# Kernel optimization log

Measured on AMD Instinct MI355X. Metric: run time of the kernel, lower is better.

The kernel has to match this reference:

```python
import jax, jax.numpy as jnp
import numpy as np
from jax import lax

CAP_SIZE = 8
N_IN, N_OUT, OUT_SIZE = 144, 10, 16
ROUTING_ITERS = 3
DN = ('NCHW', 'OIHW', 'NCHW')


def setup_inputs() -> dict:
    key = jax.random.key(0)
    ks = jax.random.split(key, 6)
    B = 2048
    inp = {
        'input': jax.random.uniform(ks[0], (B, 1, 28, 28), dtype=jnp.float32),
        'conv1_w': jax.random.normal(ks[1], (16, 1, 9, 9), dtype=jnp.float32) * 0.1,
        'conv1_b': jnp.zeros((16,), dtype=jnp.float32),
        'conv2_w': jax.random.normal(ks[2], (32, 16, 9, 9), dtype=jnp.float32) * 0.05,
        'conv2_b': jnp.zeros((32,), dtype=jnp.float32),
        'W_route': jax.random.normal(ks[3], (N_IN, N_OUT, OUT_SIZE, CAP_SIZE), dtype=jnp.float32) * 0.1,
    }
    return inp


def squash(s, axis=-1, eps=1e-8):
    sq = jnp.sum(jnp.square(s), axis=axis, keepdims=True)
    return (sq / (1.0 + sq)) * s / jnp.sqrt(sq + eps)


def reference(input, conv1_w, conv1_b, conv2_w, conv2_b, W_route):
    # PrimaryCaps: two valid convs
    x = lax.conv_general_dilated(input, conv1_w, (1, 1), 'VALID', dimension_numbers=DN)
    x = x + conv1_b[None, :, None, None]                      # [B,16,20,20]
    x = lax.conv_general_dilated(x, conv2_w, (2, 2), 'VALID', dimension_numbers=DN)
    x = x + conv2_b[None, :, None, None]                      # [B,32,6,6]
    B = x.shape[0]
    u = jnp.transpose(x.reshape(B, CAP_SIZE, -1), (0, 2, 1))  # [B,144,8]

    # prediction vectors u_hat[b,i,j,:] = W[i,j] @ u[b,i]
    u_hat = jnp.einsum('iojc,bic->bioj', W_route, u)          # [B,144,10,16]

    # routing-by-agreement
    b_log = jnp.zeros((B, N_IN, N_OUT), dtype=u_hat.dtype)
    for _ in range(ROUTING_ITERS):
        c = jax.nn.softmax(b_log, axis=2)                     # couple over out caps
        s = jnp.einsum('bio,biod->bod', c, u_hat)             # [B,10,16]
        v = squash(s)                                         # [B,10,16]
        b_log = b_log + jnp.einsum('biod,bod->bio', u_hat, v)

    pred = jnp.sqrt(jnp.sum(jnp.square(v), axis=-1))          # [B,10]
    return (pred, v)
```

## Files before the change

kernel.cpp:

```cpp
#include <hip/hip_runtime.h>


typedef _Float16 half2_t __attribute__((ext_vector_type(2)));
typedef _Float16 f16x4 __attribute__((ext_vector_type(4)));
typedef _Float16 f16x8 __attribute__((ext_vector_type(8)));
typedef float f32x16 __attribute__((ext_vector_type(16)));

static __device__ __forceinline__ float fdot2f(half2_t a, half2_t b, float c) {
#if __has_builtin(__builtin_amdgcn_fdot2)
  return __builtin_amdgcn_fdot2(a, b, c, false);
#else
  return c + (float)a[0] * (float)b[0] + (float)a[1] * (float)b[1];
#endif
}

static __device__ __forceinline__ half2_t h2(unsigned int u) {
  return __builtin_bit_cast(half2_t, u);
}

static __device__ __forceinline__ unsigned int pkh2(float a, float b) {
  half2_t h;
  h[0] = (_Float16)a;
  h[1] = (_Float16)b;
  return __builtin_bit_cast(unsigned int, h);
}

static __device__ __forceinline__ f32x16 zero16() {
  f32x16 z = {0.f, 0.f, 0.f, 0.f, 0.f, 0.f, 0.f, 0.f,
              0.f, 0.f, 0.f, 0.f, 0.f, 0.f, 0.f, 0.f};
  return z;
}

__global__ __launch_bounds__(256) void packAll(
    const float* __restrict__ w2, const float* __restrict__ Wr,
    _Float16* __restrict__ wBg, unsigned int* __restrict__ wPr) {
  int idx = blockIdx.x * 256 + threadIdx.x;
  if (idx < 92160) {
    int cp = idx & 3;
    int row = idx >> 2;
    const float* src = Wr + (size_t)row * 8 + cp * 2;
    wPr[idx] = pkh2(src[0], src[1]);
  }
  if (idx < 41472) {
    int j = idx & 7;
    int lane = (idx >> 3) & 63;
    int step = idx >> 9;
    int kh = step / 9, kw = step - kh * 9;
    int co = lane & 31, ci = (lane >> 5) * 8 + j;
    wBg[idx] = (_Float16)w2[(co * 16 + ci) * 81 + kh * 9 + kw];
  }
}

__global__ __launch_bounds__(320) void conv_fused(
    const float* __restrict__ in, const float* __restrict__ w,
    const float* __restrict__ bias1, const _Float16* __restrict__ wBg,
    const float* __restrict__ bias2, float* __restrict__ u) {
  __shared__ __align__(16) float sIn[784];
  __shared__ float sW[1296];
  __shared__ __align__(16) _Float16 sOut[8000];
  int b = blockIdx.x, t = threadIdx.x;
  const float* inb = in + b * 784;
  for (int i = t; i < 784; i += 320) sIn[i] = inb[i];
  for (int i = t; i < 1296; i += 320) sW[i] = w[i];
  __syncthreads();
  {
    int co = t / 20, oh = t % 20;
    float bv = bias1[co];
    float acc[20];
#pragma unroll
    for (int j = 0; j < 20; ++j) acc[j] = bv;
#pragma unroll
    for (int kh = 0; kh < 9; ++kh) {
      float r[28];
      const float4* row = (const float4*)&sIn[(oh + kh) * 28];
#pragma unroll
      for (int q = 0; q < 7; ++q) {
        float4 v = row[q];
        r[q * 4 + 0] = v.x; r[q * 4 + 1] = v.y; r[q * 4 + 2] = v.z; r[q * 4 + 3] = v.w;
      }
      const float* wr = &sW[co * 81 + kh * 9];
#pragma unroll
      for (int kw = 0; kw < 9; ++kw) {
        float wv = wr[kw];
#pragma unroll
        for (int j = 0; j < 20; ++j) acc[j] += wv * r[kw + j];
      }
    }
#pragma unroll
    for (int j = 0; j < 20; ++j) sOut[(oh * 20 + j) * 20 + co] = (_Float16)acc[j];
  }
  __syncthreads();

  int wv = t >> 6, lane = t & 63;
  if (wv < 2) {
    int l31 = lane & 31, half = lane >> 5;
    int r = wv * 32 + l31;
    int rc = (r < 36) ? r : 35;
    int oh = rc / 6, ow = rc - oh * 6;
    int tb = (oh * 40 + ow * 2) * 20 + half * 8;
    f32x16 acc = zero16();
    for (int kh = 0; kh < 9; ++kh) {
      int abase = tb + kh * 400;
#pragma unroll
      for (int kw = 0; kw < 9; ++kw) {
        f16x8 bf = *(const f16x8*)(wBg + ((kh * 9 + kw) * 64 + lane) * 8);
        const _Float16* ap = sOut + abase + kw * 20;
        f16x4 lo = *(const f16x4*)ap;
        f16x4 hi = *(const f16x4*)(ap + 4);
        f16x8 a = __builtin_shufflevector(lo, hi, 0, 1, 2, 3, 4, 5, 6, 7);
        acc = __builtin_amdgcn_mfma_f32_32x32x16_f16(a, bf, acc, 0, 0, 0);
      }
    }
    float bv = bias2[l31];
    int c8 = l31 >> 2;
    int ibco = (l31 & 3) * 36;
    float* ub = u + (size_t)b * 1152;
#pragma unroll
    for (int reg = 0; reg < 16; ++reg) {
      int rr = wv * 32 + (reg & 3) + 8 * (reg >> 2) + 4 * half;
      if (rr < 36) ub[(ibco + rr) * 8 + c8] = acc[reg] + bv;
    }
  }
}

__global__ __launch_bounds__(1024) void routing2_kernel(
    const float* __restrict__ u, const unsigned int* __restrict__ wPr,
    float* __restrict__ out, int B) {
  __shared__ unsigned int uhh[2][11808];
  __shared__ unsigned int ush[2][576];
  __shared__ float blog[2][1440];
  __shared__ float cc[2][1440];
  __shared__ float spart[2][960];
  __shared__ float ss[2][160];
  __shared__ float vv[2][160];
  __shared__ unsigned int vvh[2][80];
  int b0 = blockIdx.x * 2, t = threadIdx.x;
  for (int j = t; j < 1152; j += 1024) {
    int sl2 = j / 576, k = j - sl2 * 576;
    float2 p = *(const float2*)(u + (size_t)(b0 + sl2) * 1152 + k * 2);
    ush[sl2][k] = pkh2(p.x, p.y);
  }
  for (int j = t; j < 2880; j += 1024) blog[j / 1440][j % 1440] = 0.f;
  __syncthreads();

  {
    const uint4* W4 = (const uint4*)wPr;
    int idx = t;
    bool valid = idx < 11520;
    int i_ = 0, dp_ = 0;
    uint4 w0a, w1a;
    if (valid) {
      i_ = idx / 80; dp_ = idx - i_ * 80;
      int row = i_ * 160 + (dp_ >> 3) * 16 + (dp_ & 7) * 2;
      w0a = W4[row]; w1a = W4[row + 1];
    }
    while (valid) {
      int nidx = idx + 1024;
      bool nvalid = nidx < 11520;
      int ni = 0, ndp = 0;
      uint4 w0b, w1b;
      if (nvalid) {
        ni = nidx / 80; ndp = nidx - ni * 80;
        int nrow = ni * 160 + (ndp >> 3) * 16 + (ndp & 7) * 2;
        w0b = W4[nrow]; w1b = W4[nrow + 1];
      }
#pragma unroll
      for (int sl2 = 0; sl2 < 2; ++sl2) {
        const uint2* up = (const uint2*)&ush[sl2][i_ * 4];
        uint2 ua = up[0], ub = up[1];
        half2_t u0 = h2(ua.x), u1 = h2(ua.y), u2 = h2(ub.x), u3 = h2(ub.y);
        float a0 = fdot2f(h2(w0a.x), u0,
                   fdot2f(h2(w0a.y), u1,
                   fdot2f(h2(w0a.z), u2, fdot2f(h2(w0a.w), u3, 0.f))));
        float a1 = fdot2f(h2(w1a.x), u0,
                   fdot2f(h2(w1a.y), u1,
                   fdot2f(h2(w1a.z), u2, fdot2f(h2(w1a.w), u3, 0.f))));
        uhh[sl2][i_ * 82 + dp_] = pkh2(a0, a1);
      }
      idx = nidx; i_ = ni; dp_ = ndp;
      w0a = w0b; w1a = w1b;
      valid = nvalid;
    }
  }
  __syncthreads();

  int sl = t >> 9, tl = t & 511;
  for (int it = 0; it < 3; ++it) {
    if (it > 0) {
      if (tl < 144) {
        const float* br = &blog[sl][tl * 10];
        float mx = br[0];
#pragma unroll
        for (int o = 1; o < 10; ++o) mx = fmaxf(mx, br[o]);
        float e[10];
        float sum = 0.f;
#pragma unroll
        for (int o = 0; o < 10; ++o) { e[o] = __expf(br[o] - mx); sum += e[o]; }
        float inv = 1.0f / sum;
#pragma unroll
        for (int o = 0; o < 10; ++o) cc[sl][tl * 10 + o] = e[o] * inv;
      }
      __syncthreads();
    }
    if (tl < 480) {
      int ch = tl / 80, dp = tl - ch * 80;
      int o = dp >> 3;
      float a0 = 0.f, a1 = 0.f;
      int i0 = ch * 24;
      if (it == 0) {
        for (int i = i0; i < i0 + 24; ++i) {
          half2_t h = h2(uhh[sl][i * 82 + dp]);
          a0 += (float)h[0]; a1 += (float)h[1];
        }
      } else {
        for (int i = i0; i < i0 + 24; ++i) {
          float c = cc[sl][i * 10 + o];
          half2_t h = h2(uhh[sl][i * 82 + dp]);
          a0 += c * (float)h[0]; a1 += c * (float)h[1];
        }
      }
      spart[sl][ch * 160 + dp * 2] = a0;
      spart[sl][ch * 160 + dp * 2 + 1] = a1;
    }
    __syncthreads();
    if (tl < 160) {
      float s = 0.f;
#pragma unroll
      for (int ch = 0; ch < 6; ++ch) s += spart[sl][ch * 160 + tl];
      ss[sl][tl] = (it == 0) ? s * 0.1f : s;
    }
    __syncthreads();
    if (tl < 10) {
      float sq = 0.f;
#pragma unroll
      for (int d = 0; d < 16; ++d) { float x = ss[sl][tl * 16 + d]; sq += x * x; }
      float coef = (sq / (1.0f + sq)) / sqrtf(sq + 1e-8f);
#pragma unroll
      for (int q = 0; q < 8; ++q) {
        float v0 = coef * ss[sl][tl * 16 + 2 * q];
        float v1 = coef * ss[sl][tl * 16 + 2 * q + 1];
        vv[sl][tl * 16 + 2 * q] = v0;
        vv[sl][tl * 16 + 2 * q + 1] = v1;
        vvh[sl][tl * 8 + q] = pkh2(v0, v1);
      }
      if (it == 2) out[(b0 + sl) * 10 + tl] = coef * sqrtf(sq);
    }
    __syncthreads();
    if (it < 2) {
      for (int idx = t; idx < 2880; idx += 1024) {
        int s2 = idx / 1440, r = idx - s2 * 1440;
        int i = r / 10, o = r - i * 10;
        const uint2* uhp = (const uint2*)&uhh[s2][i * 82 + o * 8];
        const uint2* vp = (const uint2*)&vvh[s2][o * 8];
        float dot = 0.f;
#pragma unroll
        for (int q = 0; q < 4; ++q) {
          uint2 A = uhp[q], V = vp[q];
          dot = fdot2f(h2(A.x), h2(V.x), fdot2f(h2(A.y), h2(V.y), dot));
        }
        blog[s2][r] += dot;
      }
      __syncthreads();
    }
  }
  if (tl < 160) out[B * 10 + (b0 + sl) * 160 + tl] = vv[sl][tl];
}

extern "C" void kernel_launch(void* const* d_in, const int* in_sizes, int n_in,
                              void* d_out, int out_size, void* d_ws, size_t ws_size,
                              hipStream_t stream) {
  const float* in = (const float*)d_in[0];
  const float* w1 = (const float*)d_in[1];
  const float* b1 = (const float*)d_in[2];
  const float* w2 = (const float*)d_in[3];
  const float* b2 = (const float*)d_in[4];
  const float* Wr = (const float*)d_in[5];
  float* out = (float*)d_out;
  int B = in_sizes[0] / 784;
  float* wsf = (float*)d_ws;

  float* u = wsf;
  float* tail = wsf + (size_t)B * 1152;
  _Float16* wBg = (_Float16*)tail;
  unsigned int* wPr = (unsigned int*)(tail + 20736);

  packAll<<<360, 256, 0, stream>>>(w2, Wr, wBg, wPr);
  conv_fused<<<B, 320, 0, stream>>>(in, w1, b1, wBg, b2, u);
  routing2_kernel<<<B / 2, 1024, 0, stream>>>(u, wPr, out, B);
}
```

Before: 110.1 us.

## Fuse conv and dynamic routing into one per-sample kernel with aliased LDS

Merges the conv kernel and the routing kernel into a single kernel with one block of 320 threads per sample. The primary-capsule vector u stays in shared memory as fp16 instead of round-tripping through global memory, which removes one launch. Shared memory is one byte buffer with overlapping regions so the conv scratch is reused for the u_hat and routing arrays. In exchange, routing now runs on 320 threads per sample instead of 512, and the larger LDS footprint may limit how many blocks fit per CU.

Result: slower. 161.3 us (+46.4%).

```diff
diff --git a/kernel.cpp b/kernel.cpp
--- a/kernel.cpp
+++ b/kernel.cpp
@@ -51,18 +51,30 @@
   }
 }
 
-__global__ __launch_bounds__(320) void conv_fused(
-    const float* __restrict__ in, const float* __restrict__ w,
+__global__ __launch_bounds__(320) void capsnet_fused(
+    const float* __restrict__ in, const float* __restrict__ w1g,
     const float* __restrict__ bias1, const _Float16* __restrict__ wBg,
-    const float* __restrict__ bias2, float* __restrict__ u) {
-  __shared__ __align__(16) float sIn[784];
-  __shared__ float sW[1296];
-  __shared__ __align__(16) _Float16 sOut[8000];
+    const float* __restrict__ bias2, const unsigned int* __restrict__ wPr,
+    float* __restrict__ out, int B) {
+  __shared__ __align__(16) unsigned char smem[65216];
+  float* sIn = (float*)smem;
+  float* sW = (float*)(smem + 3136);
+  float* blog = (float*)smem;
+  float* cc = (float*)(smem + 5760);
+  _Float16* sOut = (_Float16*)(smem + 11520);
+  unsigned int* uhh = (unsigned int*)(smem + 11520);
+  _Float16* uu = (_Float16*)(smem + 58752);
+  float* spart = (float*)(smem + 61056);
+  float* ss = (float*)(smem + 63616);
+  float* vv = (float*)(smem + 64256);
+  unsigned int* vvh = (unsigned int*)(smem + 64896);
+
   int b = blockIdx.x, t = threadIdx.x;
   const float* inb = in + b * 784;
   for (int i = t; i < 784; i += 320) sIn[i] = inb[i];
-  for (int i = t; i < 1296; i += 320) sW[i] = w[i];
-  __syncthreads();
+  for (int i = t; i < 1296; i += 320) sW[i] = w1g[i];
+  __syncthreads();
+
   {
     int co = t / 20, oh = t % 20;
     float bv = bias1[co];
@@ -76,7 +88,8 @@
 #pragma unroll
       for (int q = 0; q < 7; ++q) {
         float4 v = row[q];
-        r[q * 4 + 0] = v.x; r[q * 4 + 1] = v.y; r[q * 4 + 2] = v.z; r[q * 4 + 3] = v.w;
+        r[q * 4 + 0] = v.x; r[q * 4 + 1] = v.y;
+        r[q * 4 + 2] = v.z; r[q * 4 + 3] = v.w;
       }
       const float* wr = &sW[co * 81 + kh * 9];
 #pragma unroll
@@ -114,81 +127,49 @@
     float bv = bias2[l31];
     int c8 = l31 >> 2;
     int ibco = (l31 & 3) * 36;
-    float* ub = u + (size_t)b * 1152;
 #pragma unroll
     for (int reg = 0; reg < 16; ++reg) {
       int rr = wv * 32 + (reg & 3) + 8 * (reg >> 2) + 4 * half;
-      if (rr < 36) ub[(ibco + rr) * 8 + c8] = acc[reg] + bv;
-    }
-  }
-}
-
-__global__ __launch_bounds__(1024) void routing2_kernel(
-    const float* __restrict__ u, const unsigned int* __restrict__ wPr,
-    float* __restrict__ out, int B) {
-  __shared__ unsigned int uhh[2][11808];
-  __shared__ unsigned int ush[2][576];
-  __shared__ float blog[2][1440];
-  __shared__ float cc[2][1440];
-  __shared__ float spart[2][960];
-  __shared__ float ss[2][160];
-  __shared__ float vv[2][160];
-  __shared__ unsigned int vvh[2][80];
-  int b0 = blockIdx.x * 2, t = threadIdx.x;
-  for (int j = t; j < 1152; j += 1024) {
-    int sl2 = j / 576, k = j - sl2 * 576;
-    float2 p = *(const float2*)(u + (size_t)(b0 + sl2) * 1152 + k * 2);
-    ush[sl2][k] = pkh2(p.x, p.y);
-  }
-  for (int j = t; j < 2880; j += 1024) blog[j / 1440][j % 1440] = 0.f;
+      if (rr < 36) uu[(ibco + rr) * 8 + c8] = (_Float16)(acc[reg] + bv);
+    }
+  } else {
+    for (int j = t - 128; j < 1440; j += 192) blog[j] = 0.f;
+  }
   __syncthreads();
 
   {
     const uint4* W4 = (const uint4*)wPr;
-    int idx = t;
-    bool valid = idx < 11520;
-    int i_ = 0, dp_ = 0;
-    uint4 w0a, w1a;
-    if (valid) {
-      i_ = idx / 80; dp_ = idx - i_ * 80;
-      int row = i_ * 160 + (dp_ >> 3) * 16 + (dp_ & 7) * 2;
-      w0a = W4[row]; w1a = W4[row + 1];
-    }
-    while (valid) {
-      int nidx = idx + 1024;
-      bool nvalid = nidx < 11520;
-      int ni = 0, ndp = 0;
+    int i0 = t / 80, dp = t - (t / 80) * 80;
+    int rowoff = (dp >> 3) * 16 + (dp & 7) * 2;
+    uint4 w0a = W4[i0 * 160 + rowoff];
+    uint4 w1a = W4[i0 * 160 + rowoff + 1];
+    for (int e = 0; e < 36; ++e) {
+      int i = i0 + 4 * e;
       uint4 w0b, w1b;
-      if (nvalid) {
-        ni = nidx / 80; ndp = nidx - ni * 80;
-        int nrow = ni * 160 + (ndp >> 3) * 16 + (ndp & 7) * 2;
-        w0b = W4[nrow]; w1b = W4[nrow + 1];
-      }
-#pragma unroll
-      for (int sl2 = 0; sl2 < 2; ++sl2) {
-        const uint2* up = (const uint2*)&ush[sl2][i_ * 4];
-        uint2 ua = up[0], ub = up[1];
-        half2_t u0 = h2(ua.x), u1 = h2(ua.y), u2 = h2(ub.x), u3 = h2(ub.y);
-        float a0 = fdot2f(h2(w0a.x), u0,
-                   fdot2f(h2(w0a.y), u1,
-                   fdot2f(h2(w0a.z), u2, fdot2f(h2(w0a.w), u3, 0.f))));
-        float a1 = fdot2f(h2(w1a.x), u0,
-                   fdot2f(h2(w1a.y), u1,
-                   fdot2f(h2(w1a.z), u2, fdot2f(h2(w1a.w), u3, 0.f))));
-        uhh[sl2][i_ * 82 + dp_] = pkh2(a0, a1);
-      }
-      idx = nidx; i_ = ni; dp_ = ndp;
-      w0a = w0b; w1a = w1b;
-      valid = nvalid;
-    }
-  }
-  __syncthreads();
-
-  int sl = t >> 9, tl = t & 511;
+      if (e < 35) {
+        int nr = (i + 4) * 160 + rowoff;
+        w0b = W4[nr];
+        w1b = W4[nr + 1];
+      }
+      const unsigned int* uup = (const unsigned int*)(uu + i * 8);
+      unsigned int x0 = uup[0], x1 = uup[1], x2 = uup[2], x3 = uup[3];
+      float a0 = fdot2f(h2(w0a.x), h2(x0),
+                 fdot2f(h2(w0a.y), h2(x1),
+                 fdot2f(h2(w0a.z), h2(x2), fdot2f(h2(w0a.w), h2(x3), 0.f))));
+      float a1 = fdot2f(h2(w1a.x), h2(x0),
+                 fdot2f(h2(w1a.y), h2(x1),
+                 fdot2f(h2(w1a.z), h2(x2), fdot2f(h2(w1a.w), h2(x3), 0.f))));
+      uhh[i * 82 + dp] = pkh2(a0, a1);
+      w0a = w0b;
+      w1a = w1b;
+    }
+  }
+  __syncthreads();
+
   for (int it = 0; it < 3; ++it) {
     if (it > 0) {
-      if (tl < 144) {
-        const float* br = &blog[sl][tl * 10];
+      if (t < 144) {
+        const float* br = &blog[t * 10];
         float mx = br[0];
 #pragma unroll
         for (int o = 1; o < 10; ++o) mx = fmaxf(mx, br[o]);
@@ -198,72 +179,69 @@
         for (int o = 0; o < 10; ++o) { e[o] = __expf(br[o] - mx); sum += e[o]; }
         float inv = 1.0f / sum;
 #pragma unroll
-        for (int o = 0; o < 10; ++o) cc[sl][tl * 10 + o] = e[o] * inv;
+        for (int o = 0; o < 10; ++o) cc[t * 10 + o] = e[o] * inv;
       }
       __syncthreads();
     }
-    if (tl < 480) {
-      int ch = tl / 80, dp = tl - ch * 80;
+    {
+      int ch = t / 80, dp = t - (t / 80) * 80;
       int o = dp >> 3;
+      int i0c = ch * 36;
       float a0 = 0.f, a1 = 0.f;
-      int i0 = ch * 24;
       if (it == 0) {
-        for (int i = i0; i < i0 + 24; ++i) {
-          half2_t h = h2(uhh[sl][i * 82 + dp]);
+        for (int i = i0c; i < i0c + 36; ++i) {
+          half2_t h = h2(uhh[i * 82 + dp]);
           a0 += (float)h[0]; a1 += (float)h[1];
         }
       } else {
-        for (int i = i0; i < i0 + 24; ++i) {
-          float c = cc[sl][i * 10 + o];
-          half2_t h = h2(uhh[sl][i * 82 + dp]);
+        for (int i = i0c; i < i0c + 36; ++i) {
+          float c = cc[i * 10 + o];
+          half2_t h = h2(uhh[i * 82 + dp]);
           a0 += c * (float)h[0]; a1 += c * (float)h[1];
         }
       }
-      spart[sl][ch * 160 + dp * 2] = a0;
-      spart[sl][ch * 160 + dp * 2 + 1] = a1;
+      spart[ch * 160 + dp * 2] = a0;
+      spart[ch * 160 + dp * 2 + 1] = a1;
     }
     __syncthreads();
-    if (tl < 160) {
-      float s = 0.f;
-#pragma unroll
-      for (int ch = 0; ch < 6; ++ch) s += spart[sl][ch * 160 + tl];
-      ss[sl][tl] = (it == 0) ? s * 0.1f : s;
+    if (t < 160) {
+      float s = spart[t] + spart[160 + t] + spart[320 + t] + spart[480 + t];
+      ss[t] = (it == 0) ? s * 0.1f : s;
     }
     __syncthreads();
-    if (tl < 10) {
+    if (t < 10) {
       float sq = 0.f;
 #pragma unroll
-      for (int d = 0; d < 16; ++d) { float x = ss[sl][tl * 16 + d]; sq += x * x; }
+      for (int d = 0; d < 16; ++d) { float x = ss[t * 16 + d]; sq += x * x; }
       float coef = (sq / (1.0f + sq)) / sqrtf(sq + 1e-8f);
 #pragma unroll
       for (int q = 0; q < 8; ++q) {
-        float v0 = coef * ss[sl][tl * 16 + 2 * q];
-        float v1 = coef * ss[sl][tl * 16 + 2 * q + 1];
-        vv[sl][tl * 16 + 2 * q] = v0;
-        vv[sl][tl * 16 + 2 * q + 1] = v1;
-        vvh[sl][tl * 8 + q] = pkh2(v0, v1);
-      }
-      if (it == 2) out[(b0 + sl) * 10 + tl] = coef * sqrtf(sq);
+        float v0 = coef * ss[t * 16 + 2 * q];
+        float v1 = coef * ss[t * 16 + 2 * q + 1];
+        vv[t * 16 + 2 * q] = v0;
+        vv[t * 16 + 2 * q + 1] = v1;
+        vvh[t * 8 + q] = pkh2(v0, v1);
+      }
+      if (it == 2) out[b * 10 + t] = coef * sqrtf(sq);
     }
     __syncthreads();
     if (it < 2) {
-      for (int idx = t; idx < 2880; idx += 1024) {
-        int s2 = idx / 1440, r = idx - s2 * 1440;
-        int i = r / 10, o = r - i * 10;
-        const uint2* uhp = (const uint2*)&uhh[s2][i * 82 + o * 8];
-        const uint2* vp = (const uint2*)&vvh[s2][o * 8];
+      for (int idx = t; idx < 1440; idx += 320) {
+        int i = idx / 10, o = idx - i * 10;
+        const uint2* uhp = (const uint2*)&uhh[i * 82 + o * 8];
+        const uint2* vp = (const uint2*)&vvh[o * 8];
         float dot = 0.f;
 #pragma unroll
         for (int q = 0; q < 4; ++q) {
           uint2 A = uhp[q], V = vp[q];
           dot = fdot2f(h2(A.x), h2(V.x), fdot2f(h2(A.y), h2(V.y), dot));
         }
-        blog[s2][r] += dot;
+        blog[idx] += dot;
       }
       __syncthreads();
     }
   }
-  if (tl < 160) out[B * 10 + (b0 + sl) * 160 + tl] = vv[sl][tl];
+  if (t < 160) out[B * 10 + b * 160 + t] = vv[t];
 }
 
 extern "C" void kernel_launch(void* const* d_in, const int* in_sizes, int n_in,
@@ -279,12 +257,9 @@
   int B = in_sizes[0] / 784;
   float* wsf = (float*)d_ws;
 
-  float* u = wsf;
-  float* tail = wsf + (size_t)B * 1152;
-  _Float16* wBg = (_Float16*)tail;
-  unsigned int* wPr = (unsigned int*)(tail + 20736);
+  _Float16* wBg = (_Float16*)wsf;
+  unsigned int* wPr = (unsigned int*)(wsf + 20736);
 
   packAll<<<360, 256, 0, stream>>>(w2, Wr, wBg, wPr);
-  conv_fused<<<B, 320, 0, stream>>>(in, w1, b1, wBg, b2, u);
-  routing2_kernel<<<B / 2, 1024, 0, stream>>>(u, wPr, out, B);
-}
+  capsnet_fused<<<B, 320, 0, stream>>>(in, w1, b1, wBg, b2, wPr, out, B);
+}
```

## Keep prediction vectors in registers and accumulate routing logits with LDS atomics

Applied to the files above, without the earlier changes.

The routing kernel stops materialising u_hat in shared memory (about 94 KB per block). Each of 960 threads now computes and holds 12 packed-half prediction pairs for both samples in registers, and reuses them across all three routing iterations for the weighted sums and the agreement dot products. The logit update becomes per-lane fdot2 followed by shared-memory atomicAdd, replacing the old strided loop. This cuts LDS footprint and traffic and may allow more blocks per CU, at the cost of more registers per thread and atomic contention on blog, since the 8 lanes per output capsule hit the same address.

Result: slower. 385.2 us (+249.8%).

```diff
diff --git a/kernel.cpp b/kernel.cpp
--- a/kernel.cpp
+++ b/kernel.cpp
@@ -123,147 +123,143 @@
   }
 }
 
-__global__ __launch_bounds__(1024) void routing2_kernel(
+__global__ __launch_bounds__(1024) void routing3_kernel(
     const float* __restrict__ u, const unsigned int* __restrict__ wPr,
     float* __restrict__ out, int B) {
-  __shared__ unsigned int uhh[2][11808];
   __shared__ unsigned int ush[2][576];
   __shared__ float blog[2][1440];
   __shared__ float cc[2][1440];
-  __shared__ float spart[2][960];
+  __shared__ float spart[2][12][160];
   __shared__ float ss[2][160];
   __shared__ float vv[2][160];
   __shared__ unsigned int vvh[2][80];
   int b0 = blockIdx.x * 2, t = threadIdx.x;
   for (int j = t; j < 1152; j += 1024) {
-    int sl2 = j / 576, k = j - sl2 * 576;
-    float2 p = *(const float2*)(u + (size_t)(b0 + sl2) * 1152 + k * 2);
-    ush[sl2][k] = pkh2(p.x, p.y);
+    int sl = j / 576, k = j - sl * 576;
+    float2 p = *(const float2*)(u + (size_t)(b0 + sl) * 1152 + k * 2);
+    ush[sl][k] = pkh2(p.x, p.y);
   }
   for (int j = t; j < 2880; j += 1024) blog[j / 1440][j % 1440] = 0.f;
   __syncthreads();
 
-  {
+  bool act = t < 960;
+  int ch = t / 80, dp = t - (t / 80) * 80;
+  int o = dp >> 3;
+  int rowoff = o * 16 + (dp & 7) * 2;
+  unsigned int uhA[12], uhB[12];
+  if (act) {
     const uint4* W4 = (const uint4*)wPr;
-    int idx = t;
-    bool valid = idx < 11520;
-    int i_ = 0, dp_ = 0;
-    uint4 w0a, w1a;
-    if (valid) {
-      i_ = idx / 80; dp_ = idx - i_ * 80;
-      int row = i_ * 160 + (dp_ >> 3) * 16 + (dp_ & 7) * 2;
-      w0a = W4[row]; w1a = W4[row + 1];
-    }
-    while (valid) {
-      int nidx = idx + 1024;
-      bool nvalid = nidx < 11520;
-      int ni = 0, ndp = 0;
-      uint4 w0b, w1b;
-      if (nvalid) {
-        ni = nidx / 80; ndp = nidx - ni * 80;
-        int nrow = ni * 160 + (ndp >> 3) * 16 + (ndp & 7) * 2;
-        w0b = W4[nrow]; w1b = W4[nrow + 1];
-      }
-#pragma unroll
-      for (int sl2 = 0; sl2 < 2; ++sl2) {
-        const uint2* up = (const uint2*)&ush[sl2][i_ * 4];
-        uint2 ua = up[0], ub = up[1];
-        half2_t u0 = h2(ua.x), u1 = h2(ua.y), u2 = h2(ub.x), u3 = h2(ub.y);
-        float a0 = fdot2f(h2(w0a.x), u0,
-                   fdot2f(h2(w0a.y), u1,
-                   fdot2f(h2(w0a.z), u2, fdot2f(h2(w0a.w), u3, 0.f))));
-        float a1 = fdot2f(h2(w1a.x), u0,
-                   fdot2f(h2(w1a.y), u1,
-                   fdot2f(h2(w1a.z), u2, fdot2f(h2(w1a.w), u3, 0.f))));
-        uhh[sl2][i_ * 82 + dp_] = pkh2(a0, a1);
-      }
-      idx = nidx; i_ = ni; dp_ = ndp;
-      w0a = w0b; w1a = w1b;
-      valid = nvalid;
-    }
-  }
-  __syncthreads();
-
-  int sl = t >> 9, tl = t & 511;
+#pragma unroll
+    for (int e = 0; e < 12; ++e) {
+      int i = ch * 12 + e;
+      uint4 w0 = W4[i * 160 + rowoff];
+      uint4 w1 = W4[i * 160 + rowoff + 1];
+      const uint2* upA = (const uint2*)&ush[0][i * 4];
+      const uint2* upB = (const uint2*)&ush[1][i * 4];
+      uint2 xa = upA[0], xa2 = upA[1];
+      uint2 xb = upB[0], xb2 = upB[1];
+      float p0 = fdot2f(h2(w0.x), h2(xa.x),
+                 fdot2f(h2(w0.y), h2(xa.y),
+                 fdot2f(h2(w0.z), h2(xa2.x), fdot2f(h2(w0.w), h2(xa2.y), 0.f))));
+      float p1 = fdot2f(h2(w1.x), h2(xa.x),
+                 fdot2f(h2(w1.y), h2(xa.y),
+                 fdot2f(h2(w1.z), h2(xa2.x), fdot2f(h2(w1.w), h2(xa2.y), 0.f))));
+      uhA[e] = pkh2(p0, p1);
+      float q0 = fdot2f(h2(w0.x), h2(xb.x),
+                 fdot2f(h2(w0.y), h2(xb.y),
+                 fdot2f(h2(w0.z), h2(xb2.x), fdot2f(h2(w0.w), h2(xb2.y), 0.f))));
+      float q1 = fdot2f(h2(w1.x), h2(xb.x),
+                 fdot2f(h2(w1.y), h2(xb.y),
+                 fdot2f(h2(w1.z), h2(xb2.x), fdot2f(h2(w1.w), h2(xb2.y), 0.f))));
+      uhB[e] = pkh2(q0, q1);
+    }
+  }
+
   for (int it = 0; it < 3; ++it) {
     if (it > 0) {
-      if (tl < 144) {
-        const float* br = &blog[sl][tl * 10];
+      __syncthreads();
+      if (t < 288) {
+        int sl = t / 144, i = t - sl * 144;
+        const float* br = &blog[sl][i * 10];
         float mx = br[0];
 #pragma unroll
-        for (int o = 1; o < 10; ++o) mx = fmaxf(mx, br[o]);
+        for (int oo = 1; oo < 10; ++oo) mx = fmaxf(mx, br[oo]);
         float e[10];
         float sum = 0.f;
 #pragma unroll
-        for (int o = 0; o < 10; ++o) { e[o] = __expf(br[o] - mx); sum += e[o]; }
+        for (int oo = 0; oo < 10; ++oo) { e[oo] = __expf(br[oo] - mx); sum += e[oo]; }
         float inv = 1.0f / sum;
 #pragma unroll
-        for (int o = 0; o < 10; ++o) cc[sl][tl * 10 + o] = e[o] * inv;
+        for (int oo = 0; oo < 10; ++oo) cc[sl][i * 10 + oo] = e[oo] * inv;
       }
       __syncthreads();
     }
-    if (tl < 480) {
-      int ch = tl / 80, dp = tl - ch * 80;
-      int o = dp >> 3;
-      float a0 = 0.f, a1 = 0.f;
-      int i0 = ch * 24;
+    if (act) {
+      float a0 = 0.f, a1 = 0.f, c0 = 0.f, c1 = 0.f;
       if (it == 0) {
-        for (int i = i0; i < i0 + 24; ++i) {
-          half2_t h = h2(uhh[sl][i * 82 + dp]);
-          a0 += (float)h[0]; a1 += (float)h[1];
+#pragma unroll
+        for (int e = 0; e < 12; ++e) {
+          half2_t hA = h2(uhA[e]), hB = h2(uhB[e]);
+          a0 += (float)hA[0]; a1 += (float)hA[1];
+          c0 += (float)hB[0]; c1 += (float)hB[1];
         }
       } else {
-        for (int i = i0; i < i0 + 24; ++i) {
-          float c = cc[sl][i * 10 + o];
-          half2_t h = h2(uhh[sl][i * 82 + dp]);
-          a0 += c * (float)h[0]; a1 += c * (float)h[1];
+#pragma unroll
+        for (int e = 0; e < 12; ++e) {
+          int i = ch * 12 + e;
+          float cA = cc[0][i * 10 + o];
+          float cB = cc[1][i * 10 + o];
+          half2_t hA = h2(uhA[e]), hB = h2(uhB[e]);
+          a0 += cA * (float)hA[0]; a1 += cA * (float)hA[1];
+          c0 += cB * (float)hB[0]; c1 += cB * (float)hB[1];
         }
       }
-      spart[sl][ch * 160 + dp * 2] = a0;
-      spart[sl][ch * 160 + dp * 2 + 1] = a1;
+      spart[0][ch][dp * 2] = a0; spart[0][ch][dp * 2 + 1] = a1;
+      spart[1][ch][dp * 2] = c0; spart[1][ch][dp * 2 + 1] = c1;
     }
     __syncthreads();
-    if (tl < 160) {
+    if (t < 320) {
+      int sl = t / 160, tl = t - sl * 160;
       float s = 0.f;
 #pragma unroll
-      for (int ch = 0; ch < 6; ++ch) s += spart[sl][ch * 160 + tl];
+      for (int c = 0; c < 12; ++c) s += spart[sl][c][tl];
       ss[sl][tl] = (it == 0) ? s * 0.1f : s;
     }
     __syncthreads();
-    if (tl < 10) {
+    if (t < 20) {
+      int sl = t / 10, oo = t - sl * 10;
+      const float* sr = &ss[sl][oo * 16];
       float sq = 0.f;
 #pragma unroll
-      for (int d = 0; d < 16; ++d) { float x = ss[sl][tl * 16 + d]; sq += x * x; }
+      for (int d = 0; d < 16; ++d) { float x = sr[d]; sq += x * x; }
       float coef = (sq / (1.0f + sq)) / sqrtf(sq + 1e-8f);
 #pragma unroll
       for (int q = 0; q < 8; ++q) {
-        float v0 = coef * ss[sl][tl * 16 + 2 * q];
-        float v1 = coef * ss[sl][tl * 16 + 2 * q + 1];
-        vv[sl][tl * 16 + 2 * q] = v0;
-        vv[sl][tl * 16 + 2 * q + 1] = v1;
-        vvh[sl][tl * 8 + q] = pkh2(v0, v1);
-      }
-      if (it == 2) out[(b0 + sl) * 10 + tl] = coef * sqrtf(sq);
+        float v0 = coef * sr[2 * q];
+        float v1 = coef * sr[2 * q + 1];
+        vv[sl][oo * 16 + 2 * q] = v0;
+        vv[sl][oo * 16 + 2 * q + 1] = v1;
+        vvh[sl][oo * 8 + q] = pkh2(v0, v1);
+      }
+      if (it == 2) out[(b0 + sl) * 10 + oo] = coef * sqrtf(sq);
     }
     __syncthreads();
-    if (it < 2) {
-      for (int idx = t; idx < 2880; idx += 1024) {
-        int s2 = idx / 1440, r = idx - s2 * 1440;
-        int i = r / 10, o = r - i * 10;
-        const uint2* uhp = (const uint2*)&uhh[s2][i * 82 + o * 8];
-        const uint2* vp = (const uint2*)&vvh[s2][o * 8];
-        float dot = 0.f;
-#pragma unroll
-        for (int q = 0; q < 4; ++q) {
-          uint2 A = uhp[q], V = vp[q];
-          dot = fdot2f(h2(A.x), h2(V.x), fdot2f(h2(A.y), h2(V.y), dot));
-        }
-        blog[s2][r] += dot;
-      }
-      __syncthreads();
-    }
-  }
-  if (tl < 160) out[B * 10 + (b0 + sl) * 160 + tl] = vv[sl][tl];
+    if (it < 2 && act) {
+      unsigned int vA = vvh[0][dp], vB = vvh[1][dp];
+#pragma unroll
+      for (int e = 0; e < 12; ++e) {
+        int i = ch * 12 + e;
+        float dA = fdot2f(h2(uhA[e]), h2(vA), 0.f);
+        float dB = fdot2f(h2(uhB[e]), h2(vB), 0.f);
+        atomicAdd(&blog[0][i * 10 + o], dA);
+        atomicAdd(&blog[1][i * 10 + o], dB);
+      }
+    }
+  }
+  if (t < 320) {
+    int sl = t / 160, tl = t - sl * 160;
+    out[B * 10 + (b0 + sl) * 160 + tl] = vv[sl][tl];
+  }
 }
 
 extern "C" void kernel_launch(void* const* d_in, const int* in_sizes, int n_in,
@@ -286,5 +282,5 @@
 
   packAll<<<360, 256, 0, stream>>>(w2, Wr, wBg, wPr);
   conv_fused<<<B, 320, 0, stream>>>(in, w1, b1, wBg, b2, u);
-  routing2_kernel<<<B / 2, 1024, 0, stream>>>(u, wPr, out, B);
-}
+  routing3_kernel<<<B / 2, 1024, 0, stream>>>(u, wPr, out, B);
+}
```
